# Kernel optimization log

Hardware: AMD Instinct MI355X
Metric: run time of the kernel (lower is better)

The kernel has to match this reference:

```python
import jax, jax.numpy as jnp
import numpy as np

N = 4096
HIDDEN = 256
NUM_HEADS = 8
HEAD_DIM = HIDDEN // NUM_HEADS
LN_EPS = 1e-3


def setup_inputs() -> dict:
    key = jax.random.key(0)
    ks = jax.random.split(key, 8)
    s = 1.0 / np.sqrt(HIDDEN)
    feat = jax.random.normal(ks[0], (N, HIDDEN), dtype=jnp.float32)
    Wq = jax.random.normal(ks[1], (HIDDEN, HIDDEN), dtype=jnp.float32) * s
    bq = jnp.zeros((HIDDEN,), dtype=jnp.float32)
    Wkv = jax.random.normal(ks[2], (HIDDEN, 2 * HIDDEN), dtype=jnp.float32) * s
    bkv = jnp.zeros((2 * HIDDEN,), dtype=jnp.float32)
    Weg = jax.random.normal(ks[3], (HIDDEN, 2 * NUM_HEADS), dtype=jnp.float32) * s
    beg = jnp.zeros((2 * NUM_HEADS,), dtype=jnp.float32)
    ln_g = jnp.ones((HIDDEN,), dtype=jnp.float32)
    ln_b = jnp.zeros((HIDDEN,), dtype=jnp.float32)
    return {"feat": feat, "Wq": Wq, "bq": bq, "Wkv": Wkv, "bkv": bkv,
            "Weg": Weg, "beg": beg, "ln_g": ln_g, "ln_b": ln_b}


def reference(feat, Wq, bq, Wkv, bkv, Weg, beg, ln_g, ln_b):
    n = feat.shape[0]
    # projections
    Q = feat @ Wq + bq                                  # [N, hidden]
    KV = feat @ Wkv + bkv                               # [N, 2*hidden]
    K, V = jnp.split(KV, 2, axis=-1)
    EG = feat @ Weg + beg                               # [N, 2*heads]
    E, G = jnp.split(EG, 2, axis=-1)                    # each [N, heads]
    # reshape to [N, head_dim, heads] (heads is the FAST axis, as in torch .view)
    Q = Q.reshape(n, HEAD_DIM, NUM_HEADS) * (HEAD_DIM ** -0.5)
    K = K.reshape(n, HEAD_DIM, NUM_HEADS)
    V = V.reshape(n, HEAD_DIM, NUM_HEADS)
    # all-pairs scores with per-j edge bias: [N, N, heads]
    H = jnp.einsum('idh,jdh->ijh', Q, K) + E[None, :, :]
    # softmax over i (axis 0), post-softmax sigmoid gate (per j, h)
    A = jax.nn.softmax(H, axis=0) * jax.nn.sigmoid(G)[None, :, :]
    Va = jnp.einsum('ijh,jdh->idh', A, V).reshape(n, HIDDEN)
    # layernorm eps=1e-3
    mu = jnp.mean(Va, axis=-1, keepdims=True)
    var = jnp.var(Va, axis=-1, keepdims=True)
    return (Va - mu) * jax.lax.rsqrt(var + LN_EPS) * ln_g + ln_b
```

## Files before the change

kernel.cpp:

```cpp
#include <hip/hip_runtime.h>
#include <hip/hip_bf16.h>

#define N 4096
#define HID 256
#define NH 8
#define HD 32
#define NC 784
#define CH 16
#define JSPAN (N / CH)

typedef __attribute__((ext_vector_type(8))) short short8;
typedef __attribute__((ext_vector_type(4))) short short4v;
typedef __attribute__((ext_vector_type(4))) float f32x4;
typedef __attribute__((ext_vector_type(2))) unsigned int uint2v;
typedef __attribute__((ext_vector_type(4))) unsigned int uint4v;

#define QSCALE 0.25503482f

static __device__ __forceinline__ unsigned short f2bf(float f) {
    union { float f; unsigned u; } v; v.f = f;
    unsigned r = v.u + 0x7fff + ((v.u >> 16) & 1);
    return (unsigned short)(r >> 16);
}
static __device__ __forceinline__ float bf2f(unsigned short u) {
    union { unsigned u; float f; } v; v.u = ((unsigned)u) << 16; return v.f;
}
static __device__ __forceinline__ unsigned packhu(float a, float b) {
    unsigned ua = __builtin_bit_cast(unsigned, a) + 0x8000u;
    unsigned ub = __builtin_bit_cast(unsigned, b) + 0x8000u;
    return __builtin_amdgcn_perm(ub, ua, 0x07060302u);
}

__global__ void k_prep(const float* __restrict__ feat, const float* __restrict__ Wq,
                       const float* __restrict__ Wkv, const float* __restrict__ Weg,
                       const float* __restrict__ bq, const float* __restrict__ bkv,
                       const float* __restrict__ beg, unsigned short* __restrict__ featb,
                       unsigned short* __restrict__ WbT, float* __restrict__ bC,
                       float* __restrict__ colS) {
    int bx = blockIdx.x;
    if (bx < 1024) {
        int t = bx * 256 + threadIdx.x;
        float4 v = ((const float4*)feat)[t];
        short4v o;
        o[0] = (short)f2bf(v.x); o[1] = (short)f2bf(v.y);
        o[2] = (short)f2bf(v.z); o[3] = (short)f2bf(v.w);
        ((short4v*)featb)[t] = o;
    } else {
        int c = bx - 1024, k = threadIdx.x;
        float w, b;
        if (c < 256)      { w = Wq[k * 256 + c];          b = bq[c]; }
        else if (c < 768) { w = Wkv[k * 512 + (c - 256)]; b = bkv[c - 256]; }
        else              { w = Weg[k * 16 + (c - 768)];  b = beg[c - 768]; }
        WbT[c * 256 + k] = f2bf(w);
        if (k == 0) bC[c] = b;
        if (c < 128) colS[c * 256 + k] = 0.f;
    }
}

__global__ __launch_bounds__(256) void k_proj(const unsigned short* __restrict__ featb,
                                              const unsigned short* __restrict__ WbT,
                                              const float* __restrict__ bC,
                                              unsigned short* __restrict__ Qp,
                                              unsigned short* __restrict__ Kp,
                                              unsigned short* __restrict__ VpT,
                                              float* __restrict__ sigG) {
    int w = threadIdx.x >> 6, l = threadIdx.x & 63;
    int il = l & 15, g = l >> 4;
    int c0 = blockIdx.x * 16;
    int i0 = (blockIdx.y * 4 + w) * 16;
    const short8* Arow = (const short8*)(featb + (size_t)(i0 + il) * HID);
    const short8* Brow = (const short8*)(WbT + (size_t)(c0 + il) * HID);
    f32x4 acc = {0.f, 0.f, 0.f, 0.f};
#pragma unroll
    for (int k0 = 0; k0 < HID; k0 += 32) {
        short8 a = Arow[(k0 >> 3) + g];
        short8 b = Brow[(k0 >> 3) + g];
        acc = __builtin_amdgcn_mfma_f32_16x16x32_bf16(a, b, acc, 0, 0, 0);
    }
    int c = c0 + il;
    float bias = bC[c];
#pragma unroll
    for (int r = 0; r < 4; ++r) {
        int i = i0 + g * 4 + r;
        float val = acc[r] + bias;
        if (c < 256) {
            int h = c & 7, d = c >> 3;
            Qp[((size_t)h * N + i) * HD + d] = f2bf(val * QSCALE);
        } else if (c < 512) {
            int cc = c - 256, h = cc & 7, d = cc >> 3;
            Kp[((size_t)h * N + i) * HD + d] = f2bf(val);
        } else if (c < 768) {
            int cc = c - 512, h = cc & 7, d = cc >> 3;
            VpT[((size_t)h * HD + d) * N + i] = f2bf(val);
        } else {
            int cc = c - 768;
            if (cc >= 8) sigG[(size_t)(cc - 8) * N + i] = 1.f / (1.f + __expf(-val));
        }
    }
}

__global__ __launch_bounds__(256) void k_pass1(const unsigned short* __restrict__ Qp,
                                               const unsigned short* __restrict__ Kp,
                                               float* __restrict__ colS) {
    int w = threadIdx.x >> 6, l = threadIdx.x & 63;
    int il = l & 15, g = l >> 4;
    int h = blockIdx.y;
    int j0 = (blockIdx.x * 4 + w) * 64;
    const unsigned short* Kh = Kp + (size_t)h * N * HD;
    short8 Kf[4];
#pragma unroll
    for (int t = 0; t < 4; ++t)
        Kf[t] = *(const short8*)(Kh + (size_t)(j0 + 16 * t + il) * HD + g * 8);
    const unsigned short* Qh = Qp + (size_t)h * N * HD;
    f32x4 z = {0.f, 0.f, 0.f, 0.f};
    float s[4] = {0.f, 0.f, 0.f, 0.f};
    int ibeg = blockIdx.z * 128;
    short8 Qa = *(const short8*)(Qh + (size_t)(ibeg + il) * HD + g * 8);
    short8 Qb = *(const short8*)(Qh + (size_t)(ibeg + 16 + il) * HD + g * 8);
#pragma unroll 2
    for (int it = 0; it < 4; ++it) {
        int i0 = ibeg + it * 32;
        short8 cQa = Qa, cQb = Qb;
        int in = i0 + 32;
        Qa = *(const short8*)(Qh + (size_t)(in + il) * HD + g * 8);
        Qb = *(const short8*)(Qh + (size_t)(in + 16 + il) * HD + g * 8);
        __builtin_amdgcn_sched_barrier(0);
#pragma unroll
        for (int t = 0; t < 4; ++t) {
            f32x4 Sa = __builtin_amdgcn_mfma_f32_16x16x32_bf16(cQa, Kf[t], z, 0, 0, 0);
            f32x4 Sb = __builtin_amdgcn_mfma_f32_16x16x32_bf16(cQb, Kf[t], z, 0, 0, 0);
            s[t] += ((__builtin_amdgcn_exp2f(Sa[0]) + __builtin_amdgcn_exp2f(Sa[1]))
                   + (__builtin_amdgcn_exp2f(Sa[2]) + __builtin_amdgcn_exp2f(Sa[3])))
                  + ((__builtin_amdgcn_exp2f(Sb[0]) + __builtin_amdgcn_exp2f(Sb[1]))
                   + (__builtin_amdgcn_exp2f(Sb[2]) + __builtin_amdgcn_exp2f(Sb[3])));
        }
    }
#pragma unroll
    for (int t = 0; t < 4; ++t) {
        s[t] += __shfl_xor(s[t], 16);
        s[t] += __shfl_xor(s[t], 32);
    }
    if (g == 0) {
#pragma unroll
        for (int t = 0; t < 4; ++t)
            atomicAdd(&colS[(size_t)h * N + j0 + 16 * t + il], s[t]);
    }
}

__global__ void k_vprep(unsigned short* __restrict__ VpT,
                        const float* __restrict__ sigG,
                        const float* __restrict__ colS) {
    int row = blockIdx.x >> 1;
    int j0 = ((blockIdx.x & 1) * 256 + threadIdx.x) * 8;
    int h = row >> 5;
    unsigned short* p = VpT + (size_t)row * N + j0;
    short8 v = *(short8*)p;
    const float* sg = sigG + (size_t)h * N + j0;
    const float* cs = colS + (size_t)h * N + j0;
    f32x4 sa = *(const f32x4*)sg, sb = *(const f32x4*)(sg + 4);
    f32x4 ca = *(const f32x4*)cs, cb = *(const f32x4*)(cs + 4);
    uint4v ov;
    ov[0] = packhu(bf2f((unsigned short)v[0]) * sa[0] / ca[0],
                   bf2f((unsigned short)v[1]) * sa[1] / ca[1]);
    ov[1] = packhu(bf2f((unsigned short)v[2]) * sa[2] / ca[2],
                   bf2f((unsigned short)v[3]) * sa[3] / ca[3]);
    ov[2] = packhu(bf2f((unsigned short)v[4]) * sb[0] / cb[0],
                   bf2f((unsigned short)v[5]) * sb[1] / cb[1]);
    ov[3] = packhu(bf2f((unsigned short)v[6]) * sb[2] / cb[2],
                   bf2f((unsigned short)v[7]) * sb[3] / cb[3]);
    *(uint4v*)p = ov;
}

static __device__ __forceinline__ short8 frag_dance(f32x4 Sa, f32x4 Sb) {
    unsigned A0 = packhu(__builtin_amdgcn_exp2f(Sa[0]), __builtin_amdgcn_exp2f(Sa[1]));
    unsigned A1 = packhu(__builtin_amdgcn_exp2f(Sa[2]), __builtin_amdgcn_exp2f(Sa[3]));
    unsigned B0 = packhu(__builtin_amdgcn_exp2f(Sb[0]), __builtin_amdgcn_exp2f(Sb[1]));
    unsigned B1 = packhu(__builtin_amdgcn_exp2f(Sb[2]), __builtin_amdgcn_exp2f(Sb[3]));
    uint2v r1 = __builtin_amdgcn_permlane32_swap(A0, B0, false, false);
    uint2v r2 = __builtin_amdgcn_permlane16_swap(r1[0], r1[1], false, false);
    uint2v r3 = __builtin_amdgcn_permlane32_swap(A1, B1, false, false);
    uint2v r4 = __builtin_amdgcn_permlane16_swap(r3[0], r3[1], false, false);
    uint4v pu;
    pu[0] = r2[0]; pu[1] = r4[0]; pu[2] = r2[1]; pu[3] = r4[1];
    return __builtin_bit_cast(short8, pu);
}

__global__ __launch_bounds__(128) void k_pass2(const unsigned short* __restrict__ Qp,
                                               const unsigned short* __restrict__ Kp,
                                               const unsigned short* __restrict__ VpT,
                                               unsigned short* __restrict__ Vpb) {
    int w = threadIdx.x >> 6, l = threadIdx.x & 63;
    int il = l & 15, g = l >> 4;
    int h = blockIdx.y;
    int i0 = blockIdx.x * 128 + w * 64;
    int jbeg = blockIdx.z * JSPAN;
    const unsigned short* Qh = Qp + (size_t)h * N * HD;
    const unsigned short* Kh = Kp + ((size_t)h * N + jbeg) * HD;
    const unsigned short* Vh = VpT + (size_t)h * HD * N + jbeg;
    short8 Qf[4];
#pragma unroll
    for (int q = 0; q < 4; ++q)
        Qf[q] = *(const short8*)(Qh + (size_t)(i0 + q * 16 + il) * HD + g * 8);
    f32x4 z = {0.f, 0.f, 0.f, 0.f};
    f32x4 acc[4][2];
#pragma unroll
    for (int q = 0; q < 4; ++q) { acc[q][0] = z; acc[q][1] = z; }
    short8 K0 = *(const short8*)(Kh + (size_t)il * HD + g * 8);
    short8 K1 = *(const short8*)(Kh + (size_t)(16 + il) * HD + g * 8);
    short8 V0 = *(const short8*)(Vh + (size_t)il * N + g * 8);
    short8 V1 = *(const short8*)(Vh + (size_t)(16 + il) * N + g * 8);
#pragma unroll 2
    for (int it = 0; it < 8; ++it) {
        int jb = it * 32;
        short8 cK0 = K0, cK1 = K1, cV0 = V0, cV1 = V1;
        int jn = jb + 32;
        K0 = *(const short8*)(Kh + (size_t)(jn + il) * HD + g * 8);
        K1 = *(const short8*)(Kh + (size_t)(jn + 16 + il) * HD + g * 8);
        V0 = *(const short8*)(Vh + (size_t)il * N + jn + g * 8);
        V1 = *(const short8*)(Vh + (size_t)(16 + il) * N + jn + g * 8);
        __builtin_amdgcn_sched_barrier(0);
#pragma unroll
        for (int q = 0; q < 4; ++q) {
            f32x4 SA = __builtin_amdgcn_mfma_f32_16x16x32_bf16(cK0, Qf[q], z, 0, 0, 0);
            f32x4 SB = __builtin_amdgcn_mfma_f32_16x16x32_bf16(cK1, Qf[q], z, 0, 0, 0);
            short8 Pa = frag_dance(SA, SB);
            acc[q][0] = __builtin_amdgcn_mfma_f32_16x16x32_bf16(Pa, cV0, acc[q][0], 0, 0, 0);
            acc[q][1] = __builtin_amdgcn_mfma_f32_16x16x32_bf16(Pa, cV1, acc[q][1], 0, 0, 0);
        }
    }
    unsigned short* Vout = Vpb + (size_t)(blockIdx.z * NH + h) * N * HD;
#pragma unroll
    for (int q = 0; q < 4; ++q) {
#pragma unroll
        for (int r = 0; r < 4; ++r) {
            int ia = i0 + q * 16 + g * 4 + r;
            Vout[(size_t)ia * HD + il]      = f2bf(acc[q][0][r]);
            Vout[(size_t)ia * HD + 16 + il] = f2bf(acc[q][1][r]);
        }
    }
}

__global__ __launch_bounds__(256) void k_ln(const unsigned short* __restrict__ Vpb,
                                            const float* __restrict__ gam,
                                            const float* __restrict__ bet,
                                            float* __restrict__ out) {
    int w = threadIdx.x >> 6, l = threadIdx.x & 63;
    int i = blockIdx.x * 4 + w;
    int h = l >> 3, d0 = (l & 7) << 2;
    f32x4 x = {0.f, 0.f, 0.f, 0.f};
#pragma unroll
    for (int c = 0; c < CH; ++c) {
        short4v v = *(const short4v*)(Vpb + ((size_t)(c * NH + h) * N + i) * HD + d0);
        x[0] += bf2f((unsigned short)v[0]); x[1] += bf2f((unsigned short)v[1]);
        x[2] += bf2f((unsigned short)v[2]); x[3] += bf2f((unsigned short)v[3]);
    }
    float s1 = x[0] + x[1] + x[2] + x[3];
    float s2 = x[0] * x[0] + x[1] * x[1] + x[2] * x[2] + x[3] * x[3];
#pragma unroll
    for (int off = 1; off < 64; off <<= 1) {
        s1 += __shfl_xor(s1, off);
        s2 += __shfl_xor(s2, off);
    }
    float mu = s1 * (1.f / 256.f);
    float var = s2 * (1.f / 256.f) - mu * mu;
    float rs = rsqrtf(var + 1e-3f);
#pragma unroll
    for (int r = 0; r < 4; ++r) {
        int c = (d0 + r) * 8 + h;
        out[(size_t)i * HID + c] = (x[r] - mu) * rs * gam[c] + bet[c];
    }
}

extern "C" void kernel_launch(void* const* d_in, const int* in_sizes, int n_in,
                              void* d_out, int out_size, void* d_ws, size_t ws_size,
                              hipStream_t stream) {
    const float* feat = (const float*)d_in[0];
    const float* Wq   = (const float*)d_in[1];
    const float* bq   = (const float*)d_in[2];
    const float* Wkv  = (const float*)d_in[3];
    const float* bkv  = (const float*)d_in[4];
    const float* Weg  = (const float*)d_in[5];
    const float* beg  = (const float*)d_in[6];
    const float* ln_g = (const float*)d_in[7];
    const float* ln_b = (const float*)d_in[8];
    float* out = (float*)d_out;

    char* ws = (char*)d_ws;
    unsigned short* Qp    = (unsigned short*)(ws + 0);
    unsigned short* Kp    = (unsigned short*)(ws + (2u << 20));
    unsigned short* VpT   = (unsigned short*)(ws + (4u << 20));
    unsigned short* featb = (unsigned short*)(ws + (6u << 20));
    unsigned short* WbT   = (unsigned short*)(ws + (8u << 20));
    float* bC   = (float*)(ws + (8u << 20) + (512u << 10));
    float* sigG = (float*)(ws + (8u << 20) + (528u << 10));
    float* colS = (float*)(ws + (8u << 20) + (656u << 10));
    unsigned short* Vpb = (unsigned short*)(ws + (9u << 20));

    k_prep<<<dim3(1024 + NC), 256, 0, stream>>>(feat, Wq, Wkv, Weg, bq, bkv, beg,
                                                featb, WbT, bC, colS);
    k_proj<<<dim3(49, 64), 256, 0, stream>>>(featb, WbT, bC, Qp, Kp, VpT, sigG);
    k_pass1<<<dim3(16, NH, 32), 256, 0, stream>>>(Qp, Kp, colS);
    k_vprep<<<dim3(512), 256, 0, stream>>>(VpT, sigG, colS);
    k_pass2<<<dim3(32, NH, CH), 128, 0, stream>>>(Qp, Kp, VpT, Vpb);
    k_ln<<<dim3(1024), 256, 0, stream>>>(Vpb, ln_g, ln_b, out);
}
```

Baseline: 101.3 us.

## Enlarge pass2 per-wave i-tile, deepen pass1 Q prefetch, use rcp in vprep

pass2 now gives each wave 128 query rows (8 Q fragments) instead of 64, so every K/V fragment loaded is reused twice as often, and the grid is halved to match. The j loop is fully unrolled and the MFMA section is wrapped in s_setprio. pass1 prefetches Q two steps ahead with a full unroll, and vprep swaps the per-element division for a single reciprocal multiply. The larger tile raises register pressure and halves the block count (2048 blocks of 128 threads), which may reduce occupancy.

```diff
diff --git a/kernel.cpp b/kernel.cpp
--- a/kernel.cpp
+++ b/kernel.cpp
@@ -115,15 +115,18 @@
     f32x4 z = {0.f, 0.f, 0.f, 0.f};
     float s[4] = {0.f, 0.f, 0.f, 0.f};
     int ibeg = blockIdx.z * 128;
-    short8 Qa = *(const short8*)(Qh + (size_t)(ibeg + il) * HD + g * 8);
-    short8 Qb = *(const short8*)(Qh + (size_t)(ibeg + 16 + il) * HD + g * 8);
-#pragma unroll 2
+    short8 Qa0 = *(const short8*)(Qh + (size_t)(ibeg + il) * HD + g * 8);
+    short8 Qb0 = *(const short8*)(Qh + (size_t)(ibeg + 16 + il) * HD + g * 8);
+    short8 Qa1 = *(const short8*)(Qh + (size_t)(ibeg + 32 + il) * HD + g * 8);
+    short8 Qb1 = *(const short8*)(Qh + (size_t)(ibeg + 48 + il) * HD + g * 8);
+#pragma unroll
     for (int it = 0; it < 4; ++it) {
         int i0 = ibeg + it * 32;
-        short8 cQa = Qa, cQb = Qb;
-        int in = i0 + 32;
-        Qa = *(const short8*)(Qh + (size_t)(in + il) * HD + g * 8);
-        Qb = *(const short8*)(Qh + (size_t)(in + 16 + il) * HD + g * 8);
+        short8 cQa = Qa0, cQb = Qb0;
+        Qa0 = Qa1; Qb0 = Qb1;
+        int in = i0 + 64;
+        Qa1 = *(const short8*)(Qh + (size_t)(in + il) * HD + g * 8);
+        Qb1 = *(const short8*)(Qh + (size_t)(in + 16 + il) * HD + g * 8);
         __builtin_amdgcn_sched_barrier(0);
 #pragma unroll
         for (int t = 0; t < 4; ++t) {
@@ -157,17 +160,15 @@
     short8 v = *(short8*)p;
     const float* sg = sigG + (size_t)h * N + j0;
     const float* cs = colS + (size_t)h * N + j0;
-    f32x4 sa = *(const f32x4*)sg, sb = *(const f32x4*)(sg + 4);
-    f32x4 ca = *(const f32x4*)cs, cb = *(const f32x4*)(cs + 4);
+    float sc[8];
+#pragma unroll
+    for (int k = 0; k < 8; ++k)
+        sc[k] = sg[k] * __builtin_amdgcn_rcpf(cs[k]);
     uint4v ov;
-    ov[0] = packhu(bf2f((unsigned short)v[0]) * sa[0] / ca[0],
-                   bf2f((unsigned short)v[1]) * sa[1] / ca[1]);
-    ov[1] = packhu(bf2f((unsigned short)v[2]) * sa[2] / ca[2],
-                   bf2f((unsigned short)v[3]) * sa[3] / ca[3]);
-    ov[2] = packhu(bf2f((unsigned short)v[4]) * sb[0] / cb[0],
-                   bf2f((unsigned short)v[5]) * sb[1] / cb[1]);
-    ov[3] = packhu(bf2f((unsigned short)v[6]) * sb[2] / cb[2],
-                   bf2f((unsigned short)v[7]) * sb[3] / cb[3]);
+    ov[0] = packhu(bf2f((unsigned short)v[0]) * sc[0], bf2f((unsigned short)v[1]) * sc[1]);
+    ov[1] = packhu(bf2f((unsigned short)v[2]) * sc[2], bf2f((unsigned short)v[3]) * sc[3]);
+    ov[2] = packhu(bf2f((unsigned short)v[4]) * sc[4], bf2f((unsigned short)v[5]) * sc[5]);
+    ov[3] = packhu(bf2f((unsigned short)v[6]) * sc[6], bf2f((unsigned short)v[7]) * sc[7]);
     *(uint4v*)p = ov;
 }
 
@@ -192,24 +193,24 @@
     int w = threadIdx.x >> 6, l = threadIdx.x & 63;
     int il = l & 15, g = l >> 4;
     int h = blockIdx.y;
-    int i0 = blockIdx.x * 128 + w * 64;
+    int i0 = blockIdx.x * 256 + w * 128;
     int jbeg = blockIdx.z * JSPAN;
     const unsigned short* Qh = Qp + (size_t)h * N * HD;
     const unsigned short* Kh = Kp + ((size_t)h * N + jbeg) * HD;
     const unsigned short* Vh = VpT + (size_t)h * HD * N + jbeg;
-    short8 Qf[4];
-#pragma unroll
-    for (int q = 0; q < 4; ++q)
+    short8 Qf[8];
+#pragma unroll
+    for (int q = 0; q < 8; ++q)
         Qf[q] = *(const short8*)(Qh + (size_t)(i0 + q * 16 + il) * HD + g * 8);
     f32x4 z = {0.f, 0.f, 0.f, 0.f};
-    f32x4 acc[4][2];
-#pragma unroll
-    for (int q = 0; q < 4; ++q) { acc[q][0] = z; acc[q][1] = z; }
+    f32x4 acc[8][2];
+#pragma unroll
+    for (int q = 0; q < 8; ++q) { acc[q][0] = z; acc[q][1] = z; }
     short8 K0 = *(const short8*)(Kh + (size_t)il * HD + g * 8);
     short8 K1 = *(const short8*)(Kh + (size_t)(16 + il) * HD + g * 8);
     short8 V0 = *(const short8*)(Vh + (size_t)il * N + g * 8);
     short8 V1 = *(const short8*)(Vh + (size_t)(16 + il) * N + g * 8);
-#pragma unroll 2
+#pragma unroll
     for (int it = 0; it < 8; ++it) {
         int jb = it * 32;
         short8 cK0 = K0, cK1 = K1, cV0 = V0, cV1 = V1;
@@ -219,18 +220,20 @@
         V0 = *(const short8*)(Vh + (size_t)il * N + jn + g * 8);
         V1 = *(const short8*)(Vh + (size_t)(16 + il) * N + jn + g * 8);
         __builtin_amdgcn_sched_barrier(0);
-#pragma unroll
-        for (int q = 0; q < 4; ++q) {
+        __builtin_amdgcn_s_setprio(1);
+#pragma unroll
+        for (int q = 0; q < 8; ++q) {
             f32x4 SA = __builtin_amdgcn_mfma_f32_16x16x32_bf16(cK0, Qf[q], z, 0, 0, 0);
             f32x4 SB = __builtin_amdgcn_mfma_f32_16x16x32_bf16(cK1, Qf[q], z, 0, 0, 0);
             short8 Pa = frag_dance(SA, SB);
             acc[q][0] = __builtin_amdgcn_mfma_f32_16x16x32_bf16(Pa, cV0, acc[q][0], 0, 0, 0);
             acc[q][1] = __builtin_amdgcn_mfma_f32_16x16x32_bf16(Pa, cV1, acc[q][1], 0, 0, 0);
         }
+        __builtin_amdgcn_s_setprio(0);
     }
     unsigned short* Vout = Vpb + (size_t)(blockIdx.z * NH + h) * N * HD;
 #pragma unroll
-    for (int q = 0; q < 4; ++q) {
+    for (int q = 0; q < 8; ++q) {
 #pragma unroll
         for (int r = 0; r < 4; ++r) {
             int ia = i0 + q * 16 + g * 4 + r;
@@ -301,6 +304,6 @@
     k_proj<<<dim3(49, 64), 256, 0, stream>>>(featb, WbT, bC, Qp, Kp, VpT, sigG);
     k_pass1<<<dim3(16, NH, 32), 256, 0, stream>>>(Qp, Kp, colS);
     k_vprep<<<dim3(512), 256, 0, stream>>>(VpT, sigG, colS);
-    k_pass2<<<dim3(32, NH, CH), 128, 0, stream>>>(Qp, Kp, VpT, Vpb);
+    k_pass2<<<dim3(16, NH, CH), 128, 0, stream>>>(Qp, Kp, VpT, Vpb);
     k_ln<<<dim3(1024), 256, 0, stream>>>(Vpb, ln_g, ln_b, out);
 }
```

New measurement: 99.27 us. About the same (-2.0%).
